# Optimization experiments

Measured on AMD Instinct MI355X. Metric: run time of the kernel, lower is better.

Reference implementation:

```python
import jax, jax.numpy as jnp
import numpy as np

B, D, N, H = 2, 8, 40, 128
HID = 4 * H  # 512, MLP hidden width


def setup_inputs() -> dict:
    key = jax.random.key(0)
    ks = jax.random.split(key, 12)
    s_in = 1.0 / np.sqrt(2 * H)
    s_hid = 1.0 / np.sqrt(HID)
    return {
        "node_feature": jax.random.normal(ks[0], (B, D, N, H), jnp.float32),
        "pairwise_feature": jax.random.normal(ks[1], (B, D, N, N, H), jnp.float32),
        # first MLP layer weight [2H, HID] split into node half and pairwise half
        "W1n": jax.random.uniform(ks[2], (H, HID), jnp.float32, -s_in, s_in),
        "W1p": jax.random.uniform(ks[3], (H, HID), jnp.float32, -s_in, s_in),
        "b1": jax.random.uniform(ks[4], (HID,), jnp.float32, -s_in, s_in),
        "W2": jax.random.uniform(ks[5], (HID, HID), jnp.float32, -s_hid, s_hid),
        "b2": jax.random.uniform(ks[6], (HID,), jnp.float32, -s_hid, s_hid),
        "W3": jax.random.uniform(ks[7], (HID, 1), jnp.float32, -s_hid, s_hid),
        "b3": jax.random.uniform(ks[8], (1,), jnp.float32, -s_hid, s_hid),
        "scale": jnp.float32(1.0),
        "bias": jnp.float32(0.0),
    }


def reference(node_feature, pairwise_feature, W1n, W1p, b1, W2, b2, W3, b3, scale, bias):
    # max over the dataset axis
    nf = jnp.max(node_feature, axis=-3)        # [B, N, H]
    pf = jnp.max(pairwise_feature, axis=-4)    # [B, N, N, H]
    # First linear on concat([node_expand, pair_expand]) decomposed into two
    # small projections + broadcast add (mathematically identical to
    # Linear(concat) since W1 = [W1n; W1p]).
    hn = nf @ W1n                               # [B, N, HID]
    hp = pf @ W1p                               # [B, N, N, HID]
    h = jax.nn.relu(hn[:, :, None, None, :] + hp[:, None, :, :, :] + b1)  # [B,N,N,N,HID]
    h = jax.nn.relu(h @ W2 + b2)                # [B, N, N, N, HID]
    v = h @ W3 + b3                             # [B, N, N, N, 1]
    return jax.nn.sigmoid(scale * v + bias).squeeze(-1)  # [B, N, N, N]
```

## Files before the change

kernel.cpp:

```cpp
#include <hip/hip_runtime.h>
#include <math.h>

#define BB 2
#define DD 8
#define NN 40
#define HH 128
#define HID 512
#define NJK 1600
#define MROW 64000
#define MBLK 128
#define NBLK 500

typedef __attribute__((ext_vector_type(8))) short short8;
typedef __attribute__((ext_vector_type(4))) float floatx4;

static __device__ __forceinline__ unsigned short f2bf(float x) {
    unsigned int b = __float_as_uint(x);
    b += 0x7fffu + ((b >> 16) & 1u);
    return (unsigned short)(b >> 16);
}

__global__ __launch_bounds__(256) void prep_kernel(
        const float* __restrict__ node, const float* __restrict__ pair,
        const float* __restrict__ W1n, const float* __restrict__ W1p,
        const float* __restrict__ b1, const float* __restrict__ W2,
        float* __restrict__ hp, float* __restrict__ hnb,
        unsigned short* __restrict__ w2f) {
    __shared__ float sf[2][HH];
    const int bid = blockIdx.x;
    const int t = threadIdx.x;

    if (bid < NJK) {
        int half = t >> 7, tt = t & 127;
        int row = bid*2 + half;
        int b = row / NJK, jk = row % NJK;
        float m = -INFINITY;
        #pragma unroll
        for (int d = 0; d < DD; ++d)
            m = fmaxf(m, pair[((size_t)((b*DD + d)*NJK + jk))*HH + tt]);
        sf[half][tt] = m;
        __syncthreads();
        float acc[4] = {0.f, 0.f, 0.f, 0.f};
        for (int h = 0; h < HH; ++h) {
            float v = sf[half][h];
            #pragma unroll
            for (int q = 0; q < 4; ++q)
                acc[q] = fmaf(v, W1p[h*HID + tt + q*128], acc[q]);
        }
        #pragma unroll
        for (int q = 0; q < 4; ++q)
            hp[(size_t)row*HID + tt + q*128] = acc[q];
    } else if (bid < NJK + 40) {
        int half = t >> 7, tt = t & 127;
        int row = (bid - NJK)*2 + half;
        int b = row / NN, i = row % NN;
        float m = -INFINITY;
        #pragma unroll
        for (int d = 0; d < DD; ++d)
            m = fmaxf(m, node[((size_t)((b*DD + d)*NN + i))*HH + tt]);
        sf[half][tt] = m;
        __syncthreads();
        float acc[4] = {0.f, 0.f, 0.f, 0.f};
        for (int h = 0; h < HH; ++h) {
            float v = sf[half][h];
            #pragma unroll
            for (int q = 0; q < 4; ++q)
                acc[q] = fmaf(v, W1n[h*HID + tt + q*128], acc[q]);
        }
        #pragma unroll
        for (int q = 0; q < 4; ++q)
            hnb[(size_t)row*HID + tt + q*128] = acc[q] + b1[tt + q*128];
    } else {
        int tid = (bid - (NJK + 40))*256 + t;
        int frag = tid >> 6;
        int lane = tid & 63;
        int n  = (frag >> 4)*16 + (lane & 15);
        int k0 = (frag & 15)*32 + (lane >> 4)*8;
        short8 u;
        #pragma unroll
        for (int kk = 0; kk < 8; ++kk)
            u[kk] = (short)f2bf(W2[(size_t)(k0 + kk)*HID + n]);
        *(short8*)(w2f + (size_t)tid*8) = u;
    }
}

__global__ __launch_bounds__(512, 2) void main_kernel(
        const float* __restrict__ hp, const float* __restrict__ hnb,
        const unsigned short* __restrict__ w2f,
        const float* __restrict__ b2, const float* __restrict__ W3,
        const float* __restrict__ b3, const float* __restrict__ scale,
        const float* __restrict__ bias, float* __restrict__ out) {
    __shared__ unsigned short h1s[MBLK * HID];
    const int bid = blockIdx.x;
    const int b   = bid / NBLK;
    const int m0  = (bid % NBLK) * MBLK;
    const int t   = threadIdx.x;
    char* h1c = (char*)h1s;

    const float* hpb  = hp  + (size_t)b * NJK * HID;
    const float* hnbb = hnb + (size_t)b * NN  * HID;
    #pragma unroll
    for (int it = 0; it < 16; ++it) {
        int g   = it*512 + t;
        int row = g >> 6, k8 = g & 63;
        int ig  = m0 + row;
        int i   = ig / NJK;
        int jk  = ig - i*NJK;
        const float* hr = hpb  + (size_t)jk*HID + k8*8;
        const float* nr = hnbb + (size_t)i *HID + k8*8;
        float4 p0 = *(const float4*)hr, p1 = *(const float4*)(hr + 4);
        float4 n0 = *(const float4*)nr, n1 = *(const float4*)(nr + 4);
        short8 u;
        u[0] = (short)f2bf(fmaxf(p0.x + n0.x, 0.f));
        u[1] = (short)f2bf(fmaxf(p0.y + n0.y, 0.f));
        u[2] = (short)f2bf(fmaxf(p0.z + n0.z, 0.f));
        u[3] = (short)f2bf(fmaxf(p0.w + n0.w, 0.f));
        u[4] = (short)f2bf(fmaxf(p1.x + n1.x, 0.f));
        u[5] = (short)f2bf(fmaxf(p1.y + n1.y, 0.f));
        u[6] = (short)f2bf(fmaxf(p1.z + n1.z, 0.f));
        u[7] = (short)f2bf(fmaxf(p1.w + n1.w, 0.f));
        int off = ((row << 10) + (k8 << 4)) ^ ((row & 7) << 4);
        *(short8*)(h1c + off) = u;
    }
    __syncthreads();

    const int w  = t >> 6, l = t & 63;
    const int lr = l & 15, lg = l >> 4;
    const int swz = (lr & 7) << 4;

    floatx4 acc[8][4];
    #pragma unroll
    for (int mi = 0; mi < 8; ++mi)
        #pragma unroll
        for (int tn = 0; tn < 4; ++tn)
            acc[mi][tn] = (floatx4){0.f, 0.f, 0.f, 0.f};

    const unsigned short* bbase = w2f + (size_t)w*32768 + l*8;

    short8 bcur[4];
    #pragma unroll
    for (int tn = 0; tn < 4; ++tn)
        bcur[tn] = *(const short8*)(bbase + (tn*16 + 0)*512);

    #pragma unroll 2
    for (int ks = 0; ks < 16; ++ks) {
        short8 bnxt[4];
        int ksn = (ks + 1) & 15;
        #pragma unroll
        for (int tn = 0; tn < 4; ++tn)
            bnxt[tn] = *(const short8*)(bbase + (tn*16 + ksn)*512);
        #pragma unroll
        for (int mi = 0; mi < 8; ++mi) {
            int aoff = ((((mi*16 + lr) << 10) + (ks << 6) + (lg << 4))) ^ swz;
            short8 a = *(const short8*)(h1c + aoff);
            #pragma unroll
            for (int tn = 0; tn < 4; ++tn)
                acc[mi][tn] = __builtin_amdgcn_mfma_f32_16x16x32_bf16(a, bcur[tn], acc[mi][tn], 0, 0, 0);
        }
        #pragma unroll
        for (int tn = 0; tn < 4; ++tn) bcur[tn] = bnxt[tn];
    }

    __syncthreads();
    float* red = (float*)h1s;
    float b2v[4], w3v[4];
    #pragma unroll
    for (int tn = 0; tn < 4; ++tn) {
        int col = w*64 + tn*16 + lr;
        b2v[tn] = b2[col];
        w3v[tn] = W3[col];
    }
    #pragma unroll
    for (int mi = 0; mi < 8; ++mi) {
        #pragma unroll
        for (int r = 0; r < 4; ++r) {
            float s = 0.f;
            #pragma unroll
            for (int tn = 0; tn < 4; ++tn)
                s += fmaxf(acc[mi][tn][r] + b2v[tn], 0.f) * w3v[tn];
            s += __shfl_xor(s, 1);
            s += __shfl_xor(s, 2);
            s += __shfl_xor(s, 4);
            s += __shfl_xor(s, 8);
            if (lr == 0) red[w*128 + mi*16 + lg*4 + r] = s;
        }
    }
    __syncthreads();
    if (t < MBLK) {
        float v = b3[0];
        #pragma unroll
        for (int ww = 0; ww < 8; ++ww) v += red[ww*128 + t];
        float z = scale[0]*v + bias[0];
        out[(size_t)b*MROW + m0 + t] = 1.0f / (1.0f + expf(-z));
    }
}

extern "C" void kernel_launch(void* const* d_in, const int* in_sizes, int n_in,
                              void* d_out, int out_size, void* d_ws, size_t ws_size,
                              hipStream_t stream) {
    const float* node  = (const float*)d_in[0];
    const float* pair  = (const float*)d_in[1];
    const float* W1n   = (const float*)d_in[2];
    const float* W1p   = (const float*)d_in[3];
    const float* b1    = (const float*)d_in[4];
    const float* W2    = (const float*)d_in[5];
    const float* b2    = (const float*)d_in[6];
    const float* W3    = (const float*)d_in[7];
    const float* b3    = (const float*)d_in[8];
    const float* scale = (const float*)d_in[9];
    const float* bias  = (const float*)d_in[10];
    float* out = (float*)d_out;

    float* hp = (float*)d_ws;
    float* hnb = hp + (size_t)BB*NJK*HID;
    unsigned short* w2f = (unsigned short*)(hnb + BB*NN*HID);

    hipLaunchKernelGGL(prep_kernel, dim3(NJK + 40 + 128), dim3(256), 0, stream,
                       node, pair, W1n, W1p, b1, W2, hp, hnb, w2f);
    hipLaunchKernelGGL(main_kernel, dim3(BB*NBLK), dim3(512), 0, stream,
                       hp, hnb, w2f, b2, W3, b3, scale, bias, out);
}
```

Baseline: 195.6 us.

## Retile prep projections and main GEMM with 2D i×jk tiles and 1024-thread blocks

The prep kernel now computes 16 rows per block with float4 weight loads and 8 rows per thread, reusing each W1 load across rows instead of one row per half-block. The main kernel switches to 8(i)×16(jk) output tiles, so hp rows are reused across i, and stages the 8 hnb rows in shared memory. It uses 1024 threads split into 2 row groups × 8 column waves with a 4×4 MFMA accumulator per wave, and interleaves block indices for locality. This trades the register-prefetched W2 loads for higher occupancy. The launch bound of 1024 threads with 4 blocks per CU, plus about 150KB of shared memory per block, may not be achievable and could spill registers.

```diff
diff --git a/kernel.cpp b/kernel.cpp
--- a/kernel.cpp
+++ b/kernel.cpp
@@ -8,8 +8,6 @@
 #define HID 512
 #define NJK 1600
 #define MROW 64000
-#define MBLK 128
-#define NBLK 500
 
 typedef __attribute__((ext_vector_type(8))) short short8;
 typedef __attribute__((ext_vector_type(4))) float floatx4;
@@ -26,52 +24,81 @@
         const float* __restrict__ b1, const float* __restrict__ W2,
         float* __restrict__ hp, float* __restrict__ hnb,
         unsigned short* __restrict__ w2f) {
-    __shared__ float sf[2][HH];
     const int bid = blockIdx.x;
     const int t = threadIdx.x;
 
-    if (bid < NJK) {
-        int half = t >> 7, tt = t & 127;
-        int row = bid*2 + half;
-        int b = row / NJK, jk = row % NJK;
-        float m = -INFINITY;
-        #pragma unroll
-        for (int d = 0; d < DD; ++d)
-            m = fmaxf(m, pair[((size_t)((b*DD + d)*NJK + jk))*HH + tt]);
-        sf[half][tt] = m;
+    if (bid < 200) {
+        __shared__ float pf[16][HH];
+        const int rowbase = bid * 16;
+        for (int e = t; e < 16*HH; e += 256) {
+            int r16 = e >> 7, c = e & 127;
+            int grow = rowbase + r16;
+            int b = grow / NJK, jk = grow - b*NJK;
+            float m = -INFINITY;
+            #pragma unroll
+            for (int d = 0; d < DD; ++d)
+                m = fmaxf(m, pair[((size_t)((b*DD + d)*NJK + jk))*HH + c]);
+            pf[r16][c] = m;
+        }
         __syncthreads();
-        float acc[4] = {0.f, 0.f, 0.f, 0.f};
+        const int rg = t >> 7, c4 = (t & 127) * 4;
+        float4 acc[8];
+        #pragma unroll
+        for (int r = 0; r < 8; ++r) acc[r] = make_float4(0.f,0.f,0.f,0.f);
+        #pragma unroll 4
         for (int h = 0; h < HH; ++h) {
-            float v = sf[half][h];
-            #pragma unroll
-            for (int q = 0; q < 4; ++q)
-                acc[q] = fmaf(v, W1p[h*HID + tt + q*128], acc[q]);
-        }
-        #pragma unroll
-        for (int q = 0; q < 4; ++q)
-            hp[(size_t)row*HID + tt + q*128] = acc[q];
-    } else if (bid < NJK + 40) {
-        int half = t >> 7, tt = t & 127;
-        int row = (bid - NJK)*2 + half;
-        int b = row / NN, i = row % NN;
-        float m = -INFINITY;
-        #pragma unroll
-        for (int d = 0; d < DD; ++d)
-            m = fmaxf(m, node[((size_t)((b*DD + d)*NN + i))*HH + tt]);
-        sf[half][tt] = m;
+            float4 wv = *(const float4*)&W1p[h*HID + c4];
+            #pragma unroll
+            for (int r = 0; r < 8; ++r) {
+                float pv = pf[rg*8 + r][h];
+                acc[r].x = fmaf(pv, wv.x, acc[r].x);
+                acc[r].y = fmaf(pv, wv.y, acc[r].y);
+                acc[r].z = fmaf(pv, wv.z, acc[r].z);
+                acc[r].w = fmaf(pv, wv.w, acc[r].w);
+            }
+        }
+        #pragma unroll
+        for (int r = 0; r < 8; ++r)
+            *(float4*)&hp[(size_t)(rowbase + rg*8 + r)*HID + c4] = acc[r];
+    } else if (bid < 205) {
+        __shared__ float nf[16][HH];
+        const int rowbase = (bid - 200) * 16;
+        for (int e = t; e < 16*HH; e += 256) {
+            int r16 = e >> 7, c = e & 127;
+            int grow = rowbase + r16;
+            int b = grow / NN, i = grow - b*NN;
+            float m = -INFINITY;
+            #pragma unroll
+            for (int d = 0; d < DD; ++d)
+                m = fmaxf(m, node[((size_t)((b*DD + d)*NN + i))*HH + c]);
+            nf[r16][c] = m;
+        }
         __syncthreads();
-        float acc[4] = {0.f, 0.f, 0.f, 0.f};
+        const int rg = t >> 7, c4 = (t & 127) * 4;
+        float4 acc[8];
+        #pragma unroll
+        for (int r = 0; r < 8; ++r) acc[r] = make_float4(0.f,0.f,0.f,0.f);
+        #pragma unroll 4
         for (int h = 0; h < HH; ++h) {
-            float v = sf[half][h];
-            #pragma unroll
-            for (int q = 0; q < 4; ++q)
-                acc[q] = fmaf(v, W1n[h*HID + tt + q*128], acc[q]);
-        }
-        #pragma unroll
-        for (int q = 0; q < 4; ++q)
-            hnb[(size_t)row*HID + tt + q*128] = acc[q] + b1[tt + q*128];
+            float4 wv = *(const float4*)&W1n[h*HID + c4];
+            #pragma unroll
+            for (int r = 0; r < 8; ++r) {
+                float nv = nf[rg*8 + r][h];
+                acc[r].x = fmaf(nv, wv.x, acc[r].x);
+                acc[r].y = fmaf(nv, wv.y, acc[r].y);
+                acc[r].z = fmaf(nv, wv.z, acc[r].z);
+                acc[r].w = fmaf(nv, wv.w, acc[r].w);
+            }
+        }
+        float4 b1v = *(const float4*)&b1[c4];
+        #pragma unroll
+        for (int r = 0; r < 8; ++r) {
+            float4 o = make_float4(acc[r].x + b1v.x, acc[r].y + b1v.y,
+                                   acc[r].z + b1v.z, acc[r].w + b1v.w);
+            *(float4*)&hnb[(size_t)(rowbase + rg*8 + r)*HID + c4] = o;
+        }
     } else {
-        int tid = (bid - (NJK + 40))*256 + t;
+        int tid = (bid - 205)*256 + t;
         int frag = tid >> 6;
         int lane = tid & 63;
         int n  = (frag >> 4)*16 + (lane & 15);
@@ -84,30 +111,40 @@
     }
 }
 
-__global__ __launch_bounds__(512, 2) void main_kernel(
+__global__ __launch_bounds__(1024, 4) void main_kernel(
         const float* __restrict__ hp, const float* __restrict__ hnb,
         const unsigned short* __restrict__ w2f,
         const float* __restrict__ b2, const float* __restrict__ W3,
         const float* __restrict__ b3, const float* __restrict__ scale,
         const float* __restrict__ bias, float* __restrict__ out) {
-    __shared__ unsigned short h1s[MBLK * HID];
-    const int bid = blockIdx.x;
-    const int b   = bid / NBLK;
-    const int m0  = (bid % NBLK) * MBLK;
-    const int t   = threadIdx.x;
+    __shared__ unsigned short h1s[128 * HID];
+    __shared__ float hnbs[8 * HID];
+    __shared__ float red[8][128];
+
+    const int bid  = blockIdx.x;
+    const int bid8 = (bid & 7)*125 + (bid >> 3);
+    const int b    = bid8 / 500;
+    const int rr_  = bid8 % 500;
+    const int i0   = (rr_ / 100) * 8;
+    const int jk0  = (rr_ % 100) * 16;
+    const int t    = threadIdx.x;
     char* h1c = (char*)h1s;
 
-    const float* hpb  = hp  + (size_t)b * NJK * HID;
-    const float* hnbb = hnb + (size_t)b * NN  * HID;
-    #pragma unroll
-    for (int it = 0; it < 16; ++it) {
-        int g   = it*512 + t;
+    {
+        int row = t >> 7, c4 = (t & 127) * 4;
+        *(float4*)&hnbs[row*HID + c4] =
+            *(const float4*)&hnb[(size_t)(b*NN + i0 + row)*HID + c4];
+    }
+    __syncthreads();
+
+    const float* hpb = hp + ((size_t)b*NJK + jk0)*HID;
+    #pragma unroll
+    for (int it = 0; it < 8; ++it) {
+        int g   = it*1024 + t;
         int row = g >> 6, k8 = g & 63;
-        int ig  = m0 + row;
-        int i   = ig / NJK;
-        int jk  = ig - i*NJK;
-        const float* hr = hpb  + (size_t)jk*HID + k8*8;
-        const float* nr = hnbb + (size_t)i *HID + k8*8;
+        int il  = row >> 4, jl = row & 15;
+        const float* hr = hpb + (size_t)jl*HID + k8*8;
+        const float* nr = hnbs + il*HID + k8*8;
         float4 p0 = *(const float4*)hr, p1 = *(const float4*)(hr + 4);
         float4 n0 = *(const float4*)nr, n1 = *(const float4*)(nr + 4);
         short8 u;
@@ -125,73 +162,69 @@
     __syncthreads();
 
     const int w  = t >> 6, l = t & 63;
+    const int rg = w >> 3, cw = w & 7;
     const int lr = l & 15, lg = l >> 4;
-    const int swz = (lr & 7) << 4;
-
-    floatx4 acc[8][4];
-    #pragma unroll
-    for (int mi = 0; mi < 8; ++mi)
+
+    floatx4 acc[4][4];
+    #pragma unroll
+    for (int mi = 0; mi < 4; ++mi)
         #pragma unroll
         for (int tn = 0; tn < 4; ++tn)
             acc[mi][tn] = (floatx4){0.f, 0.f, 0.f, 0.f};
 
-    const unsigned short* bbase = w2f + (size_t)w*32768 + l*8;
-
-    short8 bcur[4];
-    #pragma unroll
-    for (int tn = 0; tn < 4; ++tn)
-        bcur[tn] = *(const short8*)(bbase + (tn*16 + 0)*512);
-
-    #pragma unroll 2
+    const unsigned short* bbase = w2f + (size_t)cw*32768 + l*8;
+    const int rowb = rg*64 + lr;
+    const int swz  = (lr & 7) << 4;
+
+    #pragma unroll 1
     for (int ks = 0; ks < 16; ++ks) {
-        short8 bnxt[4];
-        int ksn = (ks + 1) & 15;
+        short8 bf[4], av[4];
         #pragma unroll
         for (int tn = 0; tn < 4; ++tn)
-            bnxt[tn] = *(const short8*)(bbase + (tn*16 + ksn)*512);
-        #pragma unroll
-        for (int mi = 0; mi < 8; ++mi) {
-            int aoff = ((((mi*16 + lr) << 10) + (ks << 6) + (lg << 4))) ^ swz;
-            short8 a = *(const short8*)(h1c + aoff);
+            bf[tn] = *(const short8*)(bbase + ((tn*16 + ks) << 9));
+        #pragma unroll
+        for (int mi = 0; mi < 4; ++mi) {
+            int aoff = (((rowb + mi*16) << 10) + (ks << 6) + (lg << 4)) ^ swz;
+            av[mi] = *(const short8*)(h1c + aoff);
+        }
+        #pragma unroll
+        for (int mi = 0; mi < 4; ++mi)
             #pragma unroll
             for (int tn = 0; tn < 4; ++tn)
-                acc[mi][tn] = __builtin_amdgcn_mfma_f32_16x16x32_bf16(a, bcur[tn], acc[mi][tn], 0, 0, 0);
-        }
-        #pragma unroll
-        for (int tn = 0; tn < 4; ++tn) bcur[tn] = bnxt[tn];
-    }
-
-    __syncthreads();
-    float* red = (float*)h1s;
+                acc[mi][tn] = __builtin_amdgcn_mfma_f32_16x16x32_bf16(av[mi], bf[tn], acc[mi][tn], 0, 0, 0);
+    }
+
     float b2v[4], w3v[4];
     #pragma unroll
     for (int tn = 0; tn < 4; ++tn) {
-        int col = w*64 + tn*16 + lr;
+        int col = cw*64 + tn*16 + lr;
         b2v[tn] = b2[col];
         w3v[tn] = W3[col];
     }
     #pragma unroll
-    for (int mi = 0; mi < 8; ++mi) {
-        #pragma unroll
-        for (int r = 0; r < 4; ++r) {
+    for (int mi = 0; mi < 4; ++mi) {
+        #pragma unroll
+        for (int q = 0; q < 4; ++q) {
             float s = 0.f;
             #pragma unroll
             for (int tn = 0; tn < 4; ++tn)
-                s += fmaxf(acc[mi][tn][r] + b2v[tn], 0.f) * w3v[tn];
+                s += fmaxf(acc[mi][tn][q] + b2v[tn], 0.f) * w3v[tn];
             s += __shfl_xor(s, 1);
             s += __shfl_xor(s, 2);
             s += __shfl_xor(s, 4);
             s += __shfl_xor(s, 8);
-            if (lr == 0) red[w*128 + mi*16 + lg*4 + r] = s;
+            if (lr == 0) red[cw][rg*64 + mi*16 + lg*4 + q] = s;
         }
     }
     __syncthreads();
-    if (t < MBLK) {
+    if (t < 128) {
         float v = b3[0];
         #pragma unroll
-        for (int ww = 0; ww < 8; ++ww) v += red[ww*128 + t];
+        for (int c = 0; c < 8; ++c) v += red[c][t];
         float z = scale[0]*v + bias[0];
-        out[(size_t)b*MROW + m0 + t] = 1.0f / (1.0f + expf(-z));
+        int il = t >> 4, jl = t & 15;
+        out[(size_t)b*MROW + (size_t)(i0 + il)*NJK + jk0 + jl] =
+            1.0f / (1.0f + expf(-z));
     }
 }
 
@@ -215,8 +248,8 @@
     float* hnb = hp + (size_t)BB*NJK*HID;
     unsigned short* w2f = (unsigned short*)(hnb + BB*NN*HID);
 
-    hipLaunchKernelGGL(prep_kernel, dim3(NJK + 40 + 128), dim3(256), 0, stream,
+    hipLaunchKernelGGL(prep_kernel, dim3(333), dim3(256), 0, stream,
                        node, pair, W1n, W1p, b1, W2, hp, hnb, w2f);
-    hipLaunchKernelGGL(main_kernel, dim3(BB*NBLK), dim3(512), 0, stream,
+    hipLaunchKernelGGL(main_kernel, dim3(1000), dim3(1024), 0, stream,
                        hp, hnb, w2f, b2, W3, b3, scale, bias, out);
 }
```

Result: faster. 184.8 us (-5.6%).
